# Kernel tuning notes

Measured on AMD Instinct MI355X. Metric: run time of the kernel, lower is better.

The kernel has to match this reference:

```python
import jax, jax.numpy as jnp
import numpy as np

B, D_IN, D_OUT = 8192, 4096, 2048

def setup_inputs() -> dict:
    key = jax.random.key(0)
    k1, k2, k3 = jax.random.split(key, 3)
    inputs = jax.random.normal(k1, (B, D_IN), dtype=jnp.float32)
    # xavier-uniform kernel
    limit = float(np.sqrt(6.0 / (D_IN + D_OUT)))
    kernel = jax.random.uniform(k2, (D_IN, D_OUT), dtype=jnp.float32, minval=-limit, maxval=limit)
    bias = jnp.zeros((D_OUT,), dtype=jnp.float32)
    map_ = jax.random.bernoulli(k3, p=0.1, shape=(D_IN, D_OUT)).astype(jnp.float32)
    return {"inputs": inputs, "kernel": kernel, "bias": bias, "map": map_}

def reference(inputs, kernel, bias, map):
    # SparseTF: mask the weight in place, then dense GEMM + bias
    masked_kernel = kernel * map            # [D_IN, D_OUT]
    out = inputs @ masked_kernel + bias     # [B, D_OUT]
    return out
```

## Files before the change

kernel.cpp:

```cpp
#include <hip/hip_runtime.h>

#define BB   8192
#define DIN  4096
#define DOUT 2048

typedef unsigned short ushort_t;
typedef __attribute__((ext_vector_type(8))) short bf16x8;
typedef __attribute__((ext_vector_type(4))) float f32x4;

__device__ inline ushort_t f2bf(float f) {
    union { float f; unsigned u; } v; v.f = f;
    unsigned u = v.u;
    return (ushort_t)((u + 0x7fffu + ((u >> 16) & 1u)) >> 16);
}

#define GLOAD16(g, s)                                                        \
    __builtin_amdgcn_global_load_lds(                                        \
        (const __attribute__((address_space(1))) void*)(g),                  \
        (__attribute__((address_space(3))) void*)(s), 16, 0, 0)

#define FENCE() asm volatile("" ::: "memory")
#define BAR()   do { FENCE(); __builtin_amdgcn_s_barrier(); FENCE(); } while (0)
#define VMCNT(n) asm volatile("s_waitcnt vmcnt(" #n ")" ::: "memory")

struct __align__(8) us4 { ushort_t x, y, z, w; };

__global__ __launch_bounds__(256) void convA(const float4* __restrict__ in,
                                             us4* __restrict__ out, int n4) {
    int i = blockIdx.x * blockDim.x + threadIdx.x;
    int stride = gridDim.x * blockDim.x;
    for (; i < n4; i += stride) {
        float4 v = in[i];
        us4 o;
        o.x = f2bf(v.x); o.y = f2bf(v.y); o.z = f2bf(v.z); o.w = f2bf(v.w);
        out[i] = o;
    }
}

__global__ __launch_bounds__(256) void maskT(const float* __restrict__ Kn,
                                             const float* __restrict__ Mp,
                                             ushort_t* __restrict__ WT) {
    __shared__ ushort_t t[32][33];
    const int n0 = blockIdx.x * 32;
    const int k0 = blockIdx.y * 32;
    const int tx = threadIdx.x, ty = threadIdx.y;
    #pragma unroll
    for (int i = ty; i < 32; i += 8) {
        size_t idx = (size_t)(k0 + i) * DOUT + (n0 + tx);
        t[i][tx] = f2bf(Kn[idx] * Mp[idx]);
    }
    __syncthreads();
    #pragma unroll
    for (int i = ty; i < 32; i += 8) {
        WT[(size_t)(n0 + i) * DIN + (k0 + tx)] = t[tx][i];
    }
}

__global__ __launch_bounds__(512) void gemm8(const ushort_t* __restrict__ A,
                                             const ushort_t* __restrict__ BT,
                                             const float* __restrict__ bias,
                                             float* __restrict__ C) {
    constexpr int K = DIN, N = DOUT;
    constexpr int NT = K / 64;
    extern __shared__ char sb[];

    const int tid  = threadIdx.x;
    const int lane = tid & 63;
    const int w    = tid >> 6;
    const int wr   = w >> 2;
    const int wcn  = w & 3;
    const int l15  = lane & 15;

    const int orig = blockIdx.y * 8 + blockIdx.x;
    const int swz  = (orig & 7) * 32 + (orig >> 3);
    const int n0   = (swz & 7) * 256;
    const int m0   = (swz >> 3) * 256;

    const int srow = lane >> 3;
    const int scol = ((lane & 7) ^ srow) * 8;
    const ushort_t* Ab = A  + (size_t)(m0 + srow) * K + scol;
    const ushort_t* Bb = BT + (size_t)(n0 + srow) * K + scol;

    auto stgA = [&](int buf, int kt, int h, int c) {
        GLOAD16(Ab + (size_t)(h * 128 + c * 8) * K + kt * 64,
                sb + buf * 65536 + h * 16384 + c * 1024);
    };
    auto stgB = [&](int buf, int kt, int h, int c) {
        GLOAD16(Bb + (size_t)(h * 128 + c * 8) * K + kt * 64,
                sb + buf * 65536 + 32768 + h * 16384 + c * 1024);
    };

    const int fxor = (l15 & 7) << 4;
    const int kq   = (lane >> 4) * 16;

    f32x4 acc[8][4] = {};
    bf16x8 bf[4][2];

    stgB(0, 0, 0, w); stgB(0, 0, 0, 8 + w);
    stgB(0, 0, 1, w); stgB(0, 0, 1, 8 + w);
    stgA(0, 0, 0, w); stgA(0, 0, 1, w);
    stgA(0, 0, 0, 8 + w); stgA(0, 0, 1, 8 + w);
    VMCNT(0);
    BAR();

    for (int t = 0; t < NT; ++t) {
        const int  cur = t & 1;
        const int  nxt = cur ^ 1;
        const bool pf  = (t + 1 < NT);
        const char* Abase = sb + cur * 65536 + wr * 16384;
        const char* Bbase = sb + cur * 65536 + 32768 + (wcn >> 1) * 16384 + (wcn & 1) * 8192;

        #pragma unroll
        for (int q = 0; q < 4; ++q) {
            bf16x8 af[2][2];
            #pragma unroll
            for (int mm = 0; mm < 2; ++mm)
                #pragma unroll
                for (int ks = 0; ks < 2; ++ks)
                    af[mm][ks] = *(const bf16x8*)(Abase + (2 * q + mm) * 2048 + l15 * 128 +
                                                  ((ks * 64 + kq) ^ fxor));
            if (q == 0) {
                #pragma unroll
                for (int n = 0; n < 4; ++n)
                    #pragma unroll
                    for (int ks = 0; ks < 2; ++ks)
                        bf[n][ks] = *(const bf16x8*)(Bbase + n * 2048 + l15 * 128 +
                                                     ((ks * 64 + kq) ^ fxor));
                if (pf) {
                    stgB(nxt, t + 1, 0, w); stgB(nxt, t + 1, 0, 8 + w);
                    stgB(nxt, t + 1, 1, w); stgB(nxt, t + 1, 1, 8 + w);
                    stgA(nxt, t + 1, 0, w); stgA(nxt, t + 1, 1, w);
                    stgA(nxt, t + 1, 0, 8 + w); stgA(nxt, t + 1, 1, 8 + w);
                }
            }
            BAR();
            __builtin_amdgcn_s_setprio(1);
            #pragma unroll
            for (int ks = 0; ks < 2; ++ks)
                #pragma unroll
                for (int mm = 0; mm < 2; ++mm)
                    #pragma unroll
                    for (int n = 0; n < 4; ++n)
                        acc[2 * q + mm][n] = __builtin_amdgcn_mfma_f32_16x16x32_bf16(
                            af[mm][ks], bf[n][ks], acc[2 * q + mm][n], 0, 0, 0);
            __builtin_amdgcn_s_setprio(0);
            if (q == 3) { VMCNT(0); }
            BAR();
        }
    }

    #pragma unroll
    for (int n = 0; n < 4; ++n) {
        const int col = n0 + wcn * 64 + n * 16 + l15;
        const float bv = bias[col];
        #pragma unroll
        for (int m = 0; m < 8; ++m) {
            const int r0 = m0 + wr * 128 + m * 16 + (lane >> 4) * 4;
            #pragma unroll
            for (int j = 0; j < 4; ++j)
                C[(size_t)(r0 + j) * N + col] = acc[m][n][j] + bv;
        }
    }
}

__global__ __launch_bounds__(1024) void gemm_fb(const float* __restrict__ A,
                                                const float* __restrict__ Kn,
                                                const float* __restrict__ Mp,
                                                const float* __restrict__ bias,
                                                float* __restrict__ C) {
    __shared__ float As[32][33];
    __shared__ float Bs[32][33];
    const int tx = threadIdx.x, ty = threadIdx.y;
    const int row = blockIdx.y * 32 + ty;
    const int col = blockIdx.x * 32 + tx;
    float acc = 0.f;
    for (int kt = 0; kt < DIN; kt += 32) {
        As[ty][tx] = A[(size_t)row * DIN + kt + tx];
        size_t bidx = (size_t)(kt + ty) * DOUT + col;
        Bs[ty][tx] = Kn[bidx] * Mp[bidx];
        __syncthreads();
        #pragma unroll
        for (int kk = 0; kk < 32; ++kk)
            acc += As[ty][kk] * Bs[kk][tx];
        __syncthreads();
    }
    C[(size_t)row * DOUT + col] = acc + bias[col];
}

extern "C" void kernel_launch(void* const* d_in, const int* in_sizes, int n_in,
                              void* d_out, int out_size, void* d_ws, size_t ws_size,
                              hipStream_t stream) {
    const float* inputs = (const float*)d_in[0];
    const float* kernel = (const float*)d_in[1];
    const float* bias   = (const float*)d_in[2];
    const float* map    = (const float*)d_in[3];
    float* out = (float*)d_out;

    const size_t abytes = (size_t)BB * DIN * sizeof(ushort_t);
    const size_t wbytes = (size_t)DIN * DOUT * sizeof(ushort_t);

    if (ws_size >= abytes + wbytes) {
        ushort_t* Abf = (ushort_t*)d_ws;
        ushort_t* WT  = (ushort_t*)((char*)d_ws + abytes);

        static bool attr_set = false;
        if (!attr_set) {
            hipFuncSetAttribute((const void*)gemm8,
                                hipFuncAttributeMaxDynamicSharedMemorySize, 131072);
            attr_set = true;
        }

        convA<<<2048, 256, 0, stream>>>((const float4*)inputs, (us4*)Abf,
                                        (int)((size_t)BB * DIN / 4));
        maskT<<<dim3(DOUT / 32, DIN / 32), dim3(32, 8), 0, stream>>>(kernel, map, WT);
        gemm8<<<dim3(DOUT / 256, BB / 256), 512, 131072, stream>>>(Abf, WT, bias, out);
    } else {
        gemm_fb<<<dim3(DOUT / 32, BB / 32), dim3(32, 32), 0, stream>>>(inputs, kernel, map,
                                                                       bias, out);
    }
}
```

Baseline: 177.4 us.

## Switch GEMM main loop to 4-stage K=32 pipeline with 3-deep prefetch

The GEMM main loop now steps K by 32 instead of 64 and keeps four LDS buffers of 32KB each, prefetching three tiles ahead with graded vmcnt waits. Before, it double-buffered 64-wide tiles and drained all loads each iteration. The aim is to hide global-load latency better and to spread A and B staging across the two compute halves. The cost is twice as many barriers per unit of K and more complex swizzled LDS addressing.

```diff
diff --git a/kernel.cpp b/kernel.cpp
--- a/kernel.cpp
+++ b/kernel.cpp
@@ -61,7 +61,7 @@
                                              const float* __restrict__ bias,
                                              float* __restrict__ C) {
     constexpr int K = DIN, N = DOUT;
-    constexpr int NT = K / 64;
+    constexpr int NT = K / 32;
     extern __shared__ char sb[];
 
     const int tid  = threadIdx.x;
@@ -76,77 +76,76 @@
     const int n0   = (swz & 7) * 256;
     const int m0   = (swz >> 3) * 256;
 
-    const int srow = lane >> 3;
-    const int scol = ((lane & 7) ^ srow) * 8;
-    const ushort_t* Ab = A  + (size_t)(m0 + srow) * K + scol;
-    const ushort_t* Bb = BT + (size_t)(n0 + srow) * K + scol;
-
-    auto stgA = [&](int buf, int kt, int h, int c) {
-        GLOAD16(Ab + (size_t)(h * 128 + c * 8) * K + kt * 64,
-                sb + buf * 65536 + h * 16384 + c * 1024);
+    const int sl  = (lane & 7) ^ (lane >> 3);
+    const int sro = (sl >> 2) * 128 + (lane >> 3);
+    const int sco = (sl & 3) * 8;
+    const ushort_t* Ab = A  + (size_t)(m0 + sro) * K + sco;
+    const ushort_t* Bb = BT + (size_t)(n0 + sro) * K + sco;
+
+    auto stgA = [&](int buf, int kt, int c) {
+        GLOAD16(Ab + (size_t)(c * 8) * K + kt * 32, sb + buf * 32768 + c * 1024);
     };
-    auto stgB = [&](int buf, int kt, int h, int c) {
-        GLOAD16(Bb + (size_t)(h * 128 + c * 8) * K + kt * 64,
-                sb + buf * 65536 + 32768 + h * 16384 + c * 1024);
+    auto stgB = [&](int buf, int kt, int c) {
+        GLOAD16(Bb + (size_t)(c * 8) * K + kt * 32, sb + buf * 32768 + 16384 + c * 1024);
     };
 
-    const int fxor = (l15 & 7) << 4;
-    const int kq   = (lane >> 4) * 16;
+    const int aslot = ((wr << 2) | (lane >> 4)) ^ (l15 & 7);
+    const int aoff  = l15 * 128 + aslot * 16;
+    const int bslot = (((wcn >> 1) << 2) | (lane >> 4)) ^ (l15 & 7);
+    const int boff  = 16384 + ((wcn & 1) * 64 + l15) * 128 + bslot * 16;
 
     f32x4 acc[8][4] = {};
-    bf16x8 bf[4][2];
-
-    stgB(0, 0, 0, w); stgB(0, 0, 0, 8 + w);
-    stgB(0, 0, 1, w); stgB(0, 0, 1, 8 + w);
-    stgA(0, 0, 0, w); stgA(0, 0, 1, w);
-    stgA(0, 0, 0, 8 + w); stgA(0, 0, 1, 8 + w);
-    VMCNT(0);
+    bf16x8 bfk[4];
+
+    #pragma unroll
+    for (int tt = 0; tt < 3; ++tt) {
+        stgA(tt, tt, w); stgA(tt, tt, 8 + w);
+        stgB(tt, tt, w); stgB(tt, tt, 8 + w);
+    }
+    VMCNT(8);
     BAR();
 
     for (int t = 0; t < NT; ++t) {
-        const int  cur = t & 1;
-        const int  nxt = cur ^ 1;
-        const bool pf  = (t + 1 < NT);
-        const char* Abase = sb + cur * 65536 + wr * 16384;
-        const char* Bbase = sb + cur * 65536 + 32768 + (wcn >> 1) * 16384 + (wcn & 1) * 8192;
-
-        #pragma unroll
-        for (int q = 0; q < 4; ++q) {
-            bf16x8 af[2][2];
+        const char* base = sb + (t & 3) * 32768;
+        const int   nb   = (t + 3) & 3;
+        const bool  pf   = (t < NT - 3);
+
+        bf16x8 af[4];
+        #pragma unroll
+        for (int mm = 0; mm < 4; ++mm)
+            af[mm] = *(const bf16x8*)(base + mm * 2048 + aoff);
+        #pragma unroll
+        for (int fn = 0; fn < 4; ++fn)
+            bfk[fn] = *(const bf16x8*)(base + fn * 2048 + boff);
+        if (pf) { stgA(nb, t + 3, w); stgA(nb, t + 3, 8 + w); }
+        BAR();
+        __builtin_amdgcn_s_setprio(1);
+        #pragma unroll
+        for (int mm = 0; mm < 4; ++mm)
             #pragma unroll
-            for (int mm = 0; mm < 2; ++mm)
-                #pragma unroll
-                for (int ks = 0; ks < 2; ++ks)
-                    af[mm][ks] = *(const bf16x8*)(Abase + (2 * q + mm) * 2048 + l15 * 128 +
-                                                  ((ks * 64 + kq) ^ fxor));
-            if (q == 0) {
-                #pragma unroll
-                for (int n = 0; n < 4; ++n)
-                    #pragma unroll
-                    for (int ks = 0; ks < 2; ++ks)
-                        bf[n][ks] = *(const bf16x8*)(Bbase + n * 2048 + l15 * 128 +
-                                                     ((ks * 64 + kq) ^ fxor));
-                if (pf) {
-                    stgB(nxt, t + 1, 0, w); stgB(nxt, t + 1, 0, 8 + w);
-                    stgB(nxt, t + 1, 1, w); stgB(nxt, t + 1, 1, 8 + w);
-                    stgA(nxt, t + 1, 0, w); stgA(nxt, t + 1, 1, w);
-                    stgA(nxt, t + 1, 0, 8 + w); stgA(nxt, t + 1, 1, 8 + w);
-                }
-            }
-            BAR();
-            __builtin_amdgcn_s_setprio(1);
+            for (int fn = 0; fn < 4; ++fn)
+                acc[mm][fn] = __builtin_amdgcn_mfma_f32_16x16x32_bf16(
+                    af[mm], bfk[fn], acc[mm][fn], 0, 0, 0);
+        __builtin_amdgcn_s_setprio(0);
+        BAR();
+
+        #pragma unroll
+        for (int mm = 0; mm < 4; ++mm)
+            af[mm] = *(const bf16x8*)(base + (4 + mm) * 2048 + aoff);
+        if (pf) { stgB(nb, t + 3, w); stgB(nb, t + 3, 8 + w); }
+        BAR();
+        __builtin_amdgcn_s_setprio(1);
+        #pragma unroll
+        for (int mm = 0; mm < 4; ++mm)
             #pragma unroll
-            for (int ks = 0; ks < 2; ++ks)
-                #pragma unroll
-                for (int mm = 0; mm < 2; ++mm)
-                    #pragma unroll
-                    for (int n = 0; n < 4; ++n)
-                        acc[2 * q + mm][n] = __builtin_amdgcn_mfma_f32_16x16x32_bf16(
-                            af[mm][ks], bf[n][ks], acc[2 * q + mm][n], 0, 0, 0);
-            __builtin_amdgcn_s_setprio(0);
-            if (q == 3) { VMCNT(0); }
-            BAR();
-        }
+            for (int fn = 0; fn < 4; ++fn)
+                acc[4 + mm][fn] = __builtin_amdgcn_mfma_f32_16x16x32_bf16(
+                    af[mm], bfk[fn], acc[4 + mm][fn], 0, 0, 0);
+        __builtin_amdgcn_s_setprio(0);
+        if (t < NT - 3)       { VMCNT(8); }
+        else if (t == NT - 3) { VMCNT(4); }
+        else if (t == NT - 2) { VMCNT(0); }
+        BAR();
     }
 
     #pragma unroll
```

Result: no change. 174.6 us (-1.6%).

## Restructure GEMM main loop into staggered A/B prefetch windows with finer quadrant MFMA

Applied to the files above, without the earlier changes.

The main loop is unrolled by two and each K-tile is split into four quadrant phases. A for the next tile and B for two tiles ahead are issued at different points across those phases, and a partial vmcnt wait replaces the full drain. This spreads the global-to-LDS loads over the compute phases so they overlap MFMA work better, and lets B loads run further ahead. In exchange the buffer reuse and wait-count logic become more delicate, the hazard window on the shared B buffer is tighter, and more fragments are held in registers.

```diff
diff --git a/kernel.cpp b/kernel.cpp
--- a/kernel.cpp
+++ b/kernel.cpp
@@ -78,76 +78,89 @@
 
     const int srow = lane >> 3;
     const int scol = ((lane & 7) ^ srow) * 8;
-    const ushort_t* Ab = A  + (size_t)(m0 + srow) * K + scol;
-    const ushort_t* Bb = BT + (size_t)(n0 + srow) * K + scol;
+    const ushort_t* Ag = A  + (size_t)(m0 + srow) * K + scol;
+    const ushort_t* Bg = BT + (size_t)(n0 + srow) * K + scol;
 
     auto stgA = [&](int buf, int kt, int h, int c) {
-        GLOAD16(Ab + (size_t)(h * 128 + c * 8) * K + kt * 64,
+        GLOAD16(Ag + (size_t)(h * 128 + c * 8) * K + kt * 64,
                 sb + buf * 65536 + h * 16384 + c * 1024);
     };
     auto stgB = [&](int buf, int kt, int h, int c) {
-        GLOAD16(Bb + (size_t)(h * 128 + c * 8) * K + kt * 64,
+        GLOAD16(Bg + (size_t)(h * 128 + c * 8) * K + kt * 64,
                 sb + buf * 65536 + 32768 + h * 16384 + c * 1024);
     };
+#define STAGE_A(BUF, KT, H) do { stgA(BUF, KT, H, w); stgA(BUF, KT, H, 8 + w); } while (0)
+#define STAGE_B(BUF, KT, H) do { stgB(BUF, KT, H, w); stgB(BUF, KT, H, 8 + w); } while (0)
 
     const int fxor = (l15 & 7) << 4;
     const int kq   = (lane >> 4) * 16;
 
     f32x4 acc[8][4] = {};
-    bf16x8 bf[4][2];
-
-    stgB(0, 0, 0, w); stgB(0, 0, 0, 8 + w);
-    stgB(0, 0, 1, w); stgB(0, 0, 1, 8 + w);
-    stgA(0, 0, 0, w); stgA(0, 0, 1, w);
-    stgA(0, 0, 0, 8 + w); stgA(0, 0, 1, 8 + w);
-    VMCNT(0);
+
+#define RD_A(BASE, DST, MOFF)                                                  \
+    _Pragma("unroll") for (int mm = 0; mm < 4; ++mm)                           \
+        _Pragma("unroll") for (int ks = 0; ks < 2; ++ks)                       \
+            DST[mm][ks] = *(const bf16x8*)((BASE) + ((MOFF) + mm) * 2048 +     \
+                                           l15 * 128 + ((ks * 64 + kq) ^ fxor));
+#define RD_B(BASE, DST, NOFF)                                                  \
+    _Pragma("unroll") for (int nn = 0; nn < 2; ++nn)                           \
+        _Pragma("unroll") for (int ks = 0; ks < 2; ++ks)                       \
+            DST[nn][ks] = *(const bf16x8*)((BASE) + ((NOFF) + nn) * 2048 +     \
+                                           l15 * 128 + ((ks * 64 + kq) ^ fxor));
+#define MFMA16(MH, BF, NB)                                                     \
+    __builtin_amdgcn_s_setprio(1);                                             \
+    _Pragma("unroll") for (int ks = 0; ks < 2; ++ks)                           \
+        _Pragma("unroll") for (int mm = 0; mm < 4; ++mm)                       \
+            _Pragma("unroll") for (int nn = 0; nn < 2; ++nn)                   \
+                acc[(MH) * 4 + mm][(NB) + nn] =                                \
+                    __builtin_amdgcn_mfma_f32_16x16x32_bf16(                   \
+                        af[mm][ks], BF[nn][ks],                                \
+                        acc[(MH) * 4 + mm][(NB) + nn], 0, 0, 0);               \
+    __builtin_amdgcn_s_setprio(0);
+
+#define WINDOW(T, P, SA, SB, WMODE)                                            \
+    {                                                                          \
+        const char* An_ = sb + (P) * 65536 + wr * 16384;                       \
+        const char* Bn_ = sb + (P) * 65536 + 32768 + (wcn >> 1) * 16384 +      \
+                          (wcn & 1) * 8192;                                    \
+        bf16x8 af[4][2], bfA[2][2], bfB[2][2];                                 \
+                                                                     \
+        RD_A(An_, af, 0);                                                      \
+        RD_B(Bn_, bfA, 0);                                                     \
+        if (SA) { STAGE_A(1 - (P), (T) + 1, 0); }                              \
+        BAR(); MFMA16(0, bfA, 0); BAR();                                       \
+                                                                     \
+        RD_B(Bn_, bfB, 2);                                                     \
+        if (SA) { STAGE_A(1 - (P), (T) + 1, 1); }                              \
+        BAR(); MFMA16(0, bfB, 2); BAR();                                       \
+                                                                     \
+        RD_A(An_, af, 4);                                                      \
+        if (SB) { STAGE_B(P, (T) + 2, 0); }                                    \
+        BAR(); MFMA16(1, bfA, 0); BAR();                                       \
+                                                                     \
+        if (SB) { STAGE_B(P, (T) + 2, 1); }                                    \
+        BAR(); MFMA16(1, bfB, 2);                                              \
+        if ((WMODE) == 4) { VMCNT(4); }                                        \
+        else if ((WMODE) == 0) { VMCNT(0); }                                   \
+        BAR();                                                                 \
+    }
+
+    STAGE_A(0, 0, 0); STAGE_A(0, 0, 1); STAGE_B(0, 0, 0); STAGE_B(0, 0, 1);
+    STAGE_B(1, 1, 0); STAGE_B(1, 1, 1);
+    VMCNT(4);
     BAR();
 
-    for (int t = 0; t < NT; ++t) {
-        const int  cur = t & 1;
-        const int  nxt = cur ^ 1;
-        const bool pf  = (t + 1 < NT);
-        const char* Abase = sb + cur * 65536 + wr * 16384;
-        const char* Bbase = sb + cur * 65536 + 32768 + (wcn >> 1) * 16384 + (wcn & 1) * 8192;
-
-        #pragma unroll
-        for (int q = 0; q < 4; ++q) {
-            bf16x8 af[2][2];
-            #pragma unroll
-            for (int mm = 0; mm < 2; ++mm)
-                #pragma unroll
-                for (int ks = 0; ks < 2; ++ks)
-                    af[mm][ks] = *(const bf16x8*)(Abase + (2 * q + mm) * 2048 + l15 * 128 +
-                                                  ((ks * 64 + kq) ^ fxor));
-            if (q == 0) {
-                #pragma unroll
-                for (int n = 0; n < 4; ++n)
-                    #pragma unroll
-                    for (int ks = 0; ks < 2; ++ks)
-                        bf[n][ks] = *(const bf16x8*)(Bbase + n * 2048 + l15 * 128 +
-                                                     ((ks * 64 + kq) ^ fxor));
-                if (pf) {
-                    stgB(nxt, t + 1, 0, w); stgB(nxt, t + 1, 0, 8 + w);
-                    stgB(nxt, t + 1, 1, w); stgB(nxt, t + 1, 1, 8 + w);
-                    stgA(nxt, t + 1, 0, w); stgA(nxt, t + 1, 1, w);
-                    stgA(nxt, t + 1, 0, 8 + w); stgA(nxt, t + 1, 1, 8 + w);
-                }
-            }
-            BAR();
-            __builtin_amdgcn_s_setprio(1);
-            #pragma unroll
-            for (int ks = 0; ks < 2; ++ks)
-                #pragma unroll
-                for (int mm = 0; mm < 2; ++mm)
-                    #pragma unroll
-                    for (int n = 0; n < 4; ++n)
-                        acc[2 * q + mm][n] = __builtin_amdgcn_mfma_f32_16x16x32_bf16(
-                            af[mm][ks], bf[n][ks], acc[2 * q + mm][n], 0, 0, 0);
-            __builtin_amdgcn_s_setprio(0);
-            if (q == 3) { VMCNT(0); }
-            BAR();
-        }
-    }
+    for (int t = 0; t < NT; t += 2) {
+        WINDOW(t, 0, (t + 1 < NT), (t + 2 < NT), (t == NT - 2) ? 0 : 4);
+        WINDOW(t + 1, 1, (t + 2 < NT), (t + 3 < NT),
+               (t + 1 == NT - 2) ? 0 : ((t + 1 < NT - 2) ? 4 : -1));
+    }
+#undef WINDOW
+#undef MFMA16
+#undef RD_A
+#undef RD_B
+#undef STAGE_A
+#undef STAGE_B
 
     #pragma unroll
     for (int n = 0; n < 4; ++n) {
```

Result: faster. 165.6 us (-6.6%).

## Restructure GEMM main loop with one barrier and interleaved LDS reads/MFMA

Applied to the files above, without the earlier changes.

Replaces the four-quarter inner loop of each k-tile, which had two barriers per quarter, with a single end-of-tile barrier. The global-to-LDS prefetch of the next tile is now issued at the top of the iteration. LDS fragment reads are split into four MFMA clusters of 16, gated by explicit lgkmcnt waits and sched_barriers, so reads for later clusters overlap earlier MFMAs. This is meant to cut barrier stalls and expose more overlap between LDS traffic and matrix instructions. In exchange it keeps more fragment registers live and relies on hand-counted lgkmcnt values matching the compiler's instruction order.

```diff
diff --git a/kernel.cpp b/kernel.cpp
--- a/kernel.cpp
+++ b/kernel.cpp
@@ -19,9 +19,11 @@
         (const __attribute__((address_space(1))) void*)(g),                  \
         (__attribute__((address_space(3))) void*)(s), 16, 0, 0)
 
-#define FENCE() asm volatile("" ::: "memory")
-#define BAR()   do { FENCE(); __builtin_amdgcn_s_barrier(); FENCE(); } while (0)
+#define FENCE()  asm volatile("" ::: "memory")
+#define BAR()    do { FENCE(); __builtin_amdgcn_s_barrier(); FENCE(); } while (0)
 #define VMCNT(n) asm volatile("s_waitcnt vmcnt(" #n ")" ::: "memory")
+#define LGKM(n)  asm volatile("s_waitcnt lgkmcnt(" #n ")" ::: "memory")
+#define SCHB()   __builtin_amdgcn_sched_barrier(0)
 
 struct __align__(8) us4 { ushort_t x, y, z, w; };
 
@@ -78,76 +80,78 @@
 
     const int srow = lane >> 3;
     const int scol = ((lane & 7) ^ srow) * 8;
-    const ushort_t* Ab = A  + (size_t)(m0 + srow) * K + scol;
-    const ushort_t* Bb = BT + (size_t)(n0 + srow) * K + scol;
+    const ushort_t* Ag = A  + (size_t)(m0 + srow) * K + scol;
+    const ushort_t* Bg = BT + (size_t)(n0 + srow) * K + scol;
 
     auto stgA = [&](int buf, int kt, int h, int c) {
-        GLOAD16(Ab + (size_t)(h * 128 + c * 8) * K + kt * 64,
+        GLOAD16(Ag + (size_t)(h * 128 + c * 8) * K + kt * 64,
                 sb + buf * 65536 + h * 16384 + c * 1024);
     };
     auto stgB = [&](int buf, int kt, int h, int c) {
-        GLOAD16(Bb + (size_t)(h * 128 + c * 8) * K + kt * 64,
+        GLOAD16(Bg + (size_t)(h * 128 + c * 8) * K + kt * 64,
                 sb + buf * 65536 + 32768 + h * 16384 + c * 1024);
     };
+#define STAGE_TILE(BUF, KT)                                                    \
+    do {                                                                       \
+        stgA(BUF, KT, 0, w); stgA(BUF, KT, 0, 8 + w);                          \
+        stgA(BUF, KT, 1, w); stgA(BUF, KT, 1, 8 + w);                          \
+        stgB(BUF, KT, 0, w); stgB(BUF, KT, 0, 8 + w);                          \
+        stgB(BUF, KT, 1, w); stgB(BUF, KT, 1, 8 + w);                          \
+    } while (0)
 
     const int fxor = (l15 & 7) << 4;
     const int kq   = (lane >> 4) * 16;
 
     f32x4 acc[8][4] = {};
-    bf16x8 bf[4][2];
-
-    stgB(0, 0, 0, w); stgB(0, 0, 0, 8 + w);
-    stgB(0, 0, 1, w); stgB(0, 0, 1, 8 + w);
-    stgA(0, 0, 0, w); stgA(0, 0, 1, w);
-    stgA(0, 0, 0, 8 + w); stgA(0, 0, 1, 8 + w);
+
+#define RDA(DST, MH, KS)                                                       \
+    _Pragma("unroll") for (int mm = 0; mm < 4; ++mm)                           \
+        DST[mm] = *(const bf16x8*)(An_ + ((MH) * 4 + mm) * 2048 + l15 * 128 +  \
+                                   (((KS) * 64 + kq) ^ fxor));
+#define RDB(DST, KS)                                                           \
+    _Pragma("unroll") for (int nn = 0; nn < 4; ++nn)                           \
+        DST[nn] = *(const bf16x8*)(Bn_ + nn * 2048 + l15 * 128 +               \
+                                   (((KS) * 64 + kq) ^ fxor));
+#define MCL(MH, AFS, BFS)                                                      \
+    __builtin_amdgcn_s_setprio(1);                                             \
+    _Pragma("unroll") for (int mm = 0; mm < 4; ++mm)                           \
+        _Pragma("unroll") for (int nn = 0; nn < 4; ++nn)                       \
+            acc[(MH) * 4 + mm][nn] = __builtin_amdgcn_mfma_f32_16x16x32_bf16(  \
+                AFS[mm], BFS[nn], acc[(MH) * 4 + mm][nn], 0, 0, 0);            \
+    __builtin_amdgcn_s_setprio(0);
+
+    STAGE_TILE(0, 0);
     VMCNT(0);
     BAR();
 
+    int cur = 0;
     for (int t = 0; t < NT; ++t) {
-        const int  cur = t & 1;
-        const int  nxt = cur ^ 1;
-        const bool pf  = (t + 1 < NT);
-        const char* Abase = sb + cur * 65536 + wr * 16384;
-        const char* Bbase = sb + cur * 65536 + 32768 + (wcn >> 1) * 16384 + (wcn & 1) * 8192;
-
-        #pragma unroll
-        for (int q = 0; q < 4; ++q) {
-            bf16x8 af[2][2];
-            #pragma unroll
-            for (int mm = 0; mm < 2; ++mm)
-                #pragma unroll
-                for (int ks = 0; ks < 2; ++ks)
-                    af[mm][ks] = *(const bf16x8*)(Abase + (2 * q + mm) * 2048 + l15 * 128 +
-                                                  ((ks * 64 + kq) ^ fxor));
-            if (q == 0) {
-                #pragma unroll
-                for (int n = 0; n < 4; ++n)
-                    #pragma unroll
-                    for (int ks = 0; ks < 2; ++ks)
-                        bf[n][ks] = *(const bf16x8*)(Bbase + n * 2048 + l15 * 128 +
-                                                     ((ks * 64 + kq) ^ fxor));
-                if (pf) {
-                    stgB(nxt, t + 1, 0, w); stgB(nxt, t + 1, 0, 8 + w);
-                    stgB(nxt, t + 1, 1, w); stgB(nxt, t + 1, 1, 8 + w);
-                    stgA(nxt, t + 1, 0, w); stgA(nxt, t + 1, 1, w);
-                    stgA(nxt, t + 1, 0, 8 + w); stgA(nxt, t + 1, 1, 8 + w);
-                }
-            }
-            BAR();
-            __builtin_amdgcn_s_setprio(1);
-            #pragma unroll
-            for (int ks = 0; ks < 2; ++ks)
-                #pragma unroll
-                for (int mm = 0; mm < 2; ++mm)
-                    #pragma unroll
-                    for (int n = 0; n < 4; ++n)
-                        acc[2 * q + mm][n] = __builtin_amdgcn_mfma_f32_16x16x32_bf16(
-                            af[mm][ks], bf[n][ks], acc[2 * q + mm][n], 0, 0, 0);
-            __builtin_amdgcn_s_setprio(0);
-            if (q == 3) { VMCNT(0); }
-            BAR();
-        }
-    }
+        const char* An_ = sb + cur * 65536 + wr * 16384;
+        const char* Bn_ = sb + cur * 65536 + 32768 + (wcn >> 1) * 16384 +
+                          (wcn & 1) * 8192;
+        const bool pf = (t + 1 < NT);
+        if (pf) STAGE_TILE(1 - cur, t + 1);
+
+        bf16x8 bf0[4], bf1[4], afA[4], afB[4];
+        RDB(bf0, 0); RDA(afA, 0, 0); RDA(afB, 1, 0);
+        LGKM(4); SCHB();
+        MCL(0, afA, bf0);
+        RDB(bf1, 1); RDA(afA, 0, 1);
+        LGKM(8); SCHB();
+        MCL(1, afB, bf0);
+        RDA(afB, 1, 1);
+        LGKM(4); SCHB();
+        MCL(0, afA, bf1);
+        LGKM(0); SCHB();
+        MCL(1, afB, bf1);
+        if (pf) { VMCNT(0); }
+        BAR();
+        cur ^= 1;
+    }
+#undef MCL
+#undef RDA
+#undef RDB
+#undef STAGE_TILE
 
     #pragma unroll
     for (int n = 0; n < 4; ++n) {
```

Measured after the change: 164.2 us. 1.08x faster.
